# Kernel optimization log

Measured on AMD Instinct MI355X. Metric: run time of the kernel, lower is better.

## Reference

```python
import jax, jax.numpy as jnp
import numpy as np

N_NODES = 50000
N_EDGES = 800000
IN_DIM = 64
OUT_DIM = 128
K = 2
FINAL_DIM = IN_DIM * (2 ** (K + 1))  # 512


def _mean_agg(h, src, dst, inv_deg, n):
    # mean over neighbors: message h[src] summed into dst, normalized by in-degree
    s = jax.ops.segment_sum(h[src], dst, num_segments=n)
    return s * inv_deg[:, None]


def setup_inputs() -> dict:
    key = jax.random.key(0)
    k1, k2, k3 = jax.random.split(key, 3)
    feature = jax.random.normal(k1, (N_NODES, IN_DIM), dtype=jnp.float32)
    edge_index = jax.random.randint(k2, (2, N_EDGES), 0, N_NODES, dtype=jnp.int64)
    W = jax.random.normal(k3, (OUT_DIM, FINAL_DIM), dtype=jnp.float32) * 0.02
    b = jnp.zeros((OUT_DIM,), dtype=jnp.float32)
    return {"feature": feature, "edge_index": edge_index, "W": W, "b": b}


def reference(feature, edge_index, W, b):
    n = feature.shape[0]
    src, dst = edge_index[0], edge_index[1]
    ones = jnp.ones((src.shape[0],), dtype=feature.dtype)
    # degree normalizers (clamped to 1) for mean aggregation, each direction
    deg_in = jax.ops.segment_sum(ones, dst, num_segments=n)
    deg_out = jax.ops.segment_sum(ones, src, num_segments=n)
    inv_in = 1.0 / jnp.maximum(deg_in, 1.0)
    inv_out = 1.0 / jnp.maximum(deg_out, 1.0)

    h = feature
    for _ in range(K + 1):  # K+1 directed hops; dim doubles each hop
        h_in = _mean_agg(h, src, dst, inv_in, n)   # aggregate from in-neighbors
        h_out = _mean_agg(h, dst, src, inv_out, n)  # aggregate from out-neighbors
        h = jnp.concatenate([h_in, h_out], axis=-1)

    # output linear projection: [N, FINAL_DIM] @ [FINAL_DIM, OUT_DIM]
    return h @ W.T + b
```

## Files before the change

### kernel.cpp

```cpp
#include <hip/hip_runtime.h>

#define NN 50000
#define NE 800000
#define NBUCK 100
#define BUCK_N 500
#define CAP 10016
#define CAPS 9024
#define PA_BLOCKS 500
#define PA_CHUNK 1600

typedef __attribute__((ext_vector_type(8))) short short8;
typedef __attribute__((ext_vector_type(4))) float floatx4;

__device__ __forceinline__ unsigned short f2b(float x) {
    unsigned u = __float_as_uint(x);
    return (unsigned short)((u + 0x7fffu + ((u >> 16) & 1u)) >> 16);
}
__device__ __forceinline__ unsigned pk2(float lo, float hi) {
    return (unsigned)f2b(lo) | ((unsigned)f2b(hi) << 16);
}
__device__ __forceinline__ float blo(unsigned u) { return __uint_as_float(u << 16); }
__device__ __forceinline__ float bhi(unsigned u) { return __uint_as_float(u & 0xffff0000u); }
__device__ __forceinline__ void acc8(uint4 u, float* a) {
    a[0] += blo(u.x); a[1] += bhi(u.x);
    a[2] += blo(u.y); a[3] += bhi(u.y);
    a[4] += blo(u.z); a[5] += bhi(u.z);
    a[6] += blo(u.w); a[7] += bhi(u.w);
}

__global__ void prep_kernel(const float4* __restrict__ f32, uint2* __restrict__ fb,
                            const float* __restrict__ W, unsigned short* __restrict__ Bnk) {
    int bid = blockIdx.x;
    if (bid < 3125) {
        int idx = bid * 256 + threadIdx.x;
        float4 v = f32[idx];
        fb[idx] = make_uint2(pk2(v.x, v.y), pk2(v.z, v.w));
    } else {
        int idx = (bid - 3125) * 256 + threadIdx.x;
        int n = idx >> 8, k = idx & 255;
        float v = (n < 128) ? W[n * 512 + k] : W[(n - 128) * 512 + 256 + k];
        Bnk[idx] = f2b(v);
    }
}

__global__ __launch_bounds__(256) void bucket_kernel(const int* __restrict__ src,
                                                     const int* __restrict__ dst,
                                                     int* __restrict__ gcnt_in,
                                                     int* __restrict__ gcnt_out,
                                                     int2* __restrict__ pin,
                                                     int2* __restrict__ pout) {
    __shared__ int cin[NBUCK], cout[NBUCK], rin[NBUCK], rout[NBUCK];
    int tid = threadIdx.x;
    if (tid < NBUCK) { cin[tid] = 0; cout[tid] = 0; }
    __syncthreads();
    int e0 = blockIdx.x * PA_CHUNK, e1 = e0 + PA_CHUNK;
    for (int e = e0 + tid; e < e1; e += 256) {
        atomicAdd(&cin[dst[e] / BUCK_N], 1);
        atomicAdd(&cout[src[e] / BUCK_N], 1);
    }
    __syncthreads();
    if (tid < NBUCK) {
        rin[tid]  = atomicAdd(&gcnt_in[tid], cin[tid]);
        rout[tid] = atomicAdd(&gcnt_out[tid], cout[tid]);
        cin[tid] = 0; cout[tid] = 0;
    }
    __syncthreads();
    for (int e = e0 + tid; e < e1; e += 256) {
        int s = src[e], d = dst[e];
        int bi = d / BUCK_N;
        int p = atomicAdd(&cin[bi], 1);
        pin[(size_t)bi * CAP + rin[bi] + p] = make_int2(d, s);
        int bo = s / BUCK_N;
        int q = atomicAdd(&cout[bo], 1);
        pout[(size_t)bo * CAP + rout[bo] + q] = make_int2(s, d);
    }
}

__global__ void bucket_scan_kernel(const int* __restrict__ gcnt_in,
                                   const int* __restrict__ gcnt_out,
                                   int* __restrict__ bb_in, int* __restrict__ bb_out) {
    if (threadIdx.x == 0) {
        int run = 0;
        for (int b = 0; b < NBUCK; ++b) { bb_in[b] = run; run += gcnt_in[b]; }
    }
    if (threadIdx.x == 1) {
        int run = 0;
        for (int b = 0; b < NBUCK; ++b) { bb_out[b] = run; run += gcnt_out[b]; }
    }
}

__global__ __launch_bounds__(1024) void csr_build_kernel(const int2* __restrict__ pin,
                                                         const int2* __restrict__ pout,
                                                         const int* __restrict__ gcnt_in,
                                                         const int* __restrict__ gcnt_out,
                                                         const int* __restrict__ bb_in,
                                                         const int* __restrict__ bb_out,
                                                         int* __restrict__ row_in,
                                                         int* __restrict__ row_out,
                                                         int* __restrict__ csr_in,
                                                         int* __restrict__ csr_out) {
    bool dirout = blockIdx.x >= NBUCK;
    int b = dirout ? blockIdx.x - NBUCK : blockIdx.x;
    const int2* pairs = (dirout ? pout : pin) + (size_t)b * CAP;
    int cnt  = dirout ? gcnt_out[b] : gcnt_in[b];
    int base = dirout ? bb_out[b] : bb_in[b];
    int* row = dirout ? row_out : row_in;
    int* csr = dirout ? csr_out : csr_in;
    int lo = b * BUCK_N;
    __shared__ unsigned sbuf[CAPS];
    __shared__ int deg[BUCK_N], incl[BUCK_N], cur[BUCK_N];
    __shared__ int hnb[NBUCK], snb[NBUCK], cnb[NBUCK];
    int tid = threadIdx.x;
    if (tid < BUCK_N) { deg[tid] = 0; cur[tid] = 0; }
    if (tid < NBUCK) { hnb[tid] = 0; cnb[tid] = 0; }
    __syncthreads();
    for (int i = tid; i < cnt; i += 1024) {
        int2 pr = pairs[i];
        atomicAdd(&deg[pr.x - lo], 1);
        atomicAdd(&hnb[pr.y / BUCK_N], 1);
    }
    __syncthreads();
    if (tid < BUCK_N) incl[tid] = deg[tid];
    if (tid < NBUCK) snb[tid] = hnb[tid];
    __syncthreads();
    for (int off = 1; off < BUCK_N; off <<= 1) {
        int v = 0, w = 0;
        if (tid < BUCK_N && tid >= off) v = incl[tid - off];
        if (tid < NBUCK && tid >= off) w = snb[tid - off];
        __syncthreads();
        if (tid < BUCK_N) incl[tid] += v;
        if (tid < NBUCK && off < NBUCK) snb[tid] += w;
        __syncthreads();
    }
    if (tid < BUCK_N) row[lo + tid] = base + incl[tid] - deg[tid];
    if (tid == 0 && b == NBUCK - 1) row[NN] = base + incl[BUCK_N - 1];
    __syncthreads();
    if (cnt <= CAPS) {
        for (int i = tid; i < cnt; i += 1024) {
            int2 pr = pairs[i];
            int nb = pr.y / BUCK_N;
            int pos = snb[nb] - hnb[nb] + atomicAdd(&cnb[nb], 1);
            sbuf[pos] = ((unsigned)(pr.x - lo) << 17) | (unsigned)pr.y;
        }
        __syncthreads();
        for (int i = tid; i < cnt; i += 1024) {
            unsigned k = sbuf[i];
            int li = k >> 17;
            int pos = atomicAdd(&cur[li], 1);
            csr[base + incl[li] - deg[li] + pos] = (int)(k & 0x1FFFFu);
        }
    } else {
        for (int i = tid; i < cnt; i += 1024) {
            int2 pr = pairs[i];
            int li = pr.x - lo;
            int pos = atomicAdd(&cur[li], 1);
            csr[base + incl[li] - deg[li] + pos] = pr.y;
        }
    }
}

__global__ void gather1_kernel(const uint4* __restrict__ feat,
                               const int* __restrict__ row_in, const int* __restrict__ csr_in,
                               const int* __restrict__ row_out, const int* __restrict__ csr_out,
                               uint4* __restrict__ h1) {
    unsigned idx = blockIdx.x * 256 + threadIdx.x;
    unsigned n = idx >> 4, r = idx & 15;
    bool is_out = (r >= 8);
    unsigned f = r & 7;
    const int* row = is_out ? row_out : row_in;
    const int* csr = is_out ? csr_out : csr_in;
    int beg = row[n], end = row[n + 1];
    float inv = 1.0f / fmaxf((float)(end - beg), 1.0f);
    float a[8] = {};
    int j = beg;
    for (; j + 3 < end; j += 4) {
        uint4 u0 = feat[(size_t)csr[j] * 8 + f];
        uint4 u1 = feat[(size_t)csr[j + 1] * 8 + f];
        uint4 u2 = feat[(size_t)csr[j + 2] * 8 + f];
        uint4 u3 = feat[(size_t)csr[j + 3] * 8 + f];
        acc8(u0, a); acc8(u1, a); acc8(u2, a); acc8(u3, a);
    }
    for (; j < end; ++j) acc8(feat[(size_t)csr[j] * 8 + f], a);
    uint4 o;
    o.x = pk2(a[0] * inv, a[1] * inv);
    o.y = pk2(a[2] * inv, a[3] * inv);
    o.z = pk2(a[4] * inv, a[5] * inv);
    o.w = pk2(a[6] * inv, a[7] * inv);
    h1[(size_t)n * 16 + r] = o;
}

__global__ void gather2_kernel(const uint4* __restrict__ h1,
                               const int* __restrict__ row_in, const int* __restrict__ csr_in,
                               const int* __restrict__ row_out, const int* __restrict__ csr_out,
                               uint4* __restrict__ h2) {
    unsigned idx = blockIdx.x * 256 + threadIdx.x;
    unsigned n = idx >> 5, r = idx & 31;
    bool is_out = (r >= 16);
    unsigned f = r & 15;
    const int* row = is_out ? row_out : row_in;
    const int* csr = is_out ? csr_out : csr_in;
    int beg = row[n], end = row[n + 1];
    float inv = 1.0f / fmaxf((float)(end - beg), 1.0f);
    float a[8] = {};
    int j = beg;
    for (; j + 3 < end; j += 4) {
        uint4 u0 = h1[(size_t)csr[j] * 16 + f];
        uint4 u1 = h1[(size_t)csr[j + 1] * 16 + f];
        uint4 u2 = h1[(size_t)csr[j + 2] * 16 + f];
        uint4 u3 = h1[(size_t)csr[j + 3] * 16 + f];
        acc8(u0, a); acc8(u1, a); acc8(u2, a); acc8(u3, a);
    }
    for (; j < end; ++j) acc8(h1[(size_t)csr[j] * 16 + f], a);
    uint4 o;
    o.x = pk2(a[0] * inv, a[1] * inv);
    o.y = pk2(a[2] * inv, a[3] * inv);
    o.z = pk2(a[4] * inv, a[5] * inv);
    o.w = pk2(a[6] * inv, a[7] * inv);
    h2[(size_t)n * 32 + r] = o;
}

__global__ __launch_bounds__(256) void gemm_mfma_kernel(const unsigned short* __restrict__ A,
                                                        const unsigned short* __restrict__ Bnk,
                                                        unsigned short* __restrict__ C) {
    __shared__ unsigned short Bs[16][264];
    __shared__ unsigned short Cb[4][16][264];
    int tid = threadIdx.x;
    int wave = tid >> 6, lane = tid & 63;
    int l15 = lane & 15, q = lane >> 4;
    int m0 = blockIdx.x * 128;
    short8 af[2][8];
#pragma unroll
    for (int t = 0; t < 2; ++t) {
        int mrow = m0 + (wave + 4 * t) * 16 + l15;
        const unsigned short* Arow = A + (size_t)min(mrow, NN - 1) * 256;
#pragma unroll
        for (int s = 0; s < 8; ++s)
            af[t][s] = *(const short8*)(Arow + s * 32 + q * 8);
    }
    floatx4 acc[2][16];
#pragma unroll
    for (int t = 0; t < 2; ++t)
#pragma unroll
        for (int c = 0; c < 16; ++c) acc[t][c] = (floatx4){0.f, 0.f, 0.f, 0.f};
#pragma unroll
    for (int c = 0; c < 16; ++c) {
        {
            int nl = tid >> 4, seg = tid & 15;
            const uint4* srcp = (const uint4*)(Bnk + ((size_t)(16 * c + nl)) * 256 + seg * 16);
            uint4 v0 = srcp[0], v1 = srcp[1];
            *(uint4*)&Bs[nl][seg * 16] = v0;
            *(uint4*)&Bs[nl][seg * 16 + 8] = v1;
        }
        __syncthreads();
#pragma unroll
        for (int s = 0; s < 8; ++s) {
            short8 bf = *(const short8*)&Bs[l15][s * 32 + q * 8];
            acc[0][c] = __builtin_amdgcn_mfma_f32_16x16x32_bf16(af[0][s], bf, acc[0][c], 0, 0, 0);
            acc[1][c] = __builtin_amdgcn_mfma_f32_16x16x32_bf16(af[1][s], bf, acc[1][c], 0, 0, 0);
        }
        __syncthreads();
    }
#pragma unroll
    for (int t = 0; t < 2; ++t) {
#pragma unroll
        for (int c = 0; c < 16; ++c)
#pragma unroll
            for (int r = 0; r < 4; ++r)
                Cb[wave][q * 4 + r][16 * c + l15] = f2b(acc[t][c][r]);
        __syncthreads();
#pragma unroll
        for (int i = 0; i < 8; ++i) {
            int tt = i * 64 + lane;
            int rrow = tt >> 5;
            int seg = tt & 31;
            int m = m0 + (wave + 4 * t) * 16 + rrow;
            if (m < NN) {
                uint4 v = *(const uint4*)&Cb[wave][rrow][seg * 8];
                *(uint4*)(C + (size_t)m * 256 + seg * 8) = v;
            }
        }
        __syncthreads();
    }
}

__global__ void final_kernel(const uint4* __restrict__ g,
                             const int* __restrict__ row_in, const int* __restrict__ csr_in,
                             const int* __restrict__ row_out, const int* __restrict__ csr_out,
                             const float4* __restrict__ b4, float4* __restrict__ out) {
    unsigned idx = blockIdx.x * 256 + threadIdx.x;
    unsigned n = idx >> 4, f = idx & 15;
    float a[8] = {};
    {
        int beg = row_in[n], end = row_in[n + 1];
        float inv = 1.0f / fmaxf((float)(end - beg), 1.0f);
        float s[8] = {};
        int j = beg;
        for (; j + 3 < end; j += 4) {
            uint4 u0 = g[(size_t)csr_in[j] * 32 + f];
            uint4 u1 = g[(size_t)csr_in[j + 1] * 32 + f];
            uint4 u2 = g[(size_t)csr_in[j + 2] * 32 + f];
            uint4 u3 = g[(size_t)csr_in[j + 3] * 32 + f];
            acc8(u0, s); acc8(u1, s); acc8(u2, s); acc8(u3, s);
        }
        for (; j < end; ++j) acc8(g[(size_t)csr_in[j] * 32 + f], s);
#pragma unroll
        for (int i = 0; i < 8; ++i) a[i] += s[i] * inv;
    }
    {
        int beg = row_out[n], end = row_out[n + 1];
        float inv = 1.0f / fmaxf((float)(end - beg), 1.0f);
        float s[8] = {};
        int j = beg;
        for (; j + 3 < end; j += 4) {
            uint4 u0 = g[(size_t)csr_out[j] * 32 + 16 + f];
            uint4 u1 = g[(size_t)csr_out[j + 1] * 32 + 16 + f];
            uint4 u2 = g[(size_t)csr_out[j + 2] * 32 + 16 + f];
            uint4 u3 = g[(size_t)csr_out[j + 3] * 32 + 16 + f];
            acc8(u0, s); acc8(u1, s); acc8(u2, s); acc8(u3, s);
        }
        for (; j < end; ++j) acc8(g[(size_t)csr_out[j] * 32 + 16 + f], s);
#pragma unroll
        for (int i = 0; i < 8; ++i) a[i] += s[i] * inv;
    }
    float4 b0 = b4[2 * f], b1 = b4[2 * f + 1];
    out[(size_t)n * 32 + 2 * f]     = make_float4(a[0] + b0.x, a[1] + b0.y, a[2] + b0.z, a[3] + b0.w);
    out[(size_t)n * 32 + 2 * f + 1] = make_float4(a[4] + b1.x, a[5] + b1.y, a[6] + b1.z, a[7] + b1.w);
}

extern "C" void kernel_launch(void* const* d_in, const int* in_sizes, int n_in,
                              void* d_out, int out_size, void* d_ws, size_t ws_size,
                              hipStream_t stream) {
    const float* feature = (const float*)d_in[0];
    const int*   edges   = (const int*)d_in[1];
    const float* W       = (const float*)d_in[2];
    const float* b       = (const float*)d_in[3];
    const int* src = edges;
    const int* dst = edges + NE;
    float* out = (float*)d_out;

    unsigned short* featb = (unsigned short*)d_ws;
    unsigned short* h1b = featb + (size_t)NN * 64;
    unsigned short* h2b = h1b + (size_t)NN * 128;
    unsigned short* gb  = h2b + (size_t)NN * 256;
    unsigned short* Bnk = gb + (size_t)NN * 256;
    int2* pin  = (int2*)(Bnk + 65536);
    int2* pout = pin + (size_t)NBUCK * CAP;
    int* csr_in  = (int*)(pout + (size_t)NBUCK * CAP);
    int* csr_out = csr_in + NE;
    int* row_in  = csr_out + NE;
    int* row_out = row_in + NN + 1;
    int* gcnt_in  = row_out + NN + 1;
    int* gcnt_out = gcnt_in + 128;
    int* bb_in   = gcnt_out + 128;
    int* bb_out  = bb_in + 128;

    (void)hipMemsetAsync(gcnt_in, 0, 256 * sizeof(int), stream);
    prep_kernel<<<3125 + 256, 256, 0, stream>>>((const float4*)feature, (uint2*)featb, W, Bnk);
    bucket_kernel<<<PA_BLOCKS, 256, 0, stream>>>(src, dst, gcnt_in, gcnt_out, pin, pout);
    bucket_scan_kernel<<<1, 64, 0, stream>>>(gcnt_in, gcnt_out, bb_in, bb_out);
    csr_build_kernel<<<2 * NBUCK, 1024, 0, stream>>>(pin, pout, gcnt_in, gcnt_out,
                                                     bb_in, bb_out, row_in, row_out,
                                                     csr_in, csr_out);

    gather1_kernel<<<(NN * 16) / 256, 256, 0, stream>>>(
        (const uint4*)featb, row_in, csr_in, row_out, csr_out, (uint4*)h1b);
    gather2_kernel<<<(NN * 32) / 256, 256, 0, stream>>>(
        (const uint4*)h1b, row_in, csr_in, row_out, csr_out, (uint4*)h2b);
    gemm_mfma_kernel<<<(NN + 127) / 128, 256, 0, stream>>>(h2b, Bnk, gb);
    final_kernel<<<(NN * 16) / 256, 256, 0, stream>>>(
        (const uint4*)gb, row_in, csr_in, row_out, csr_out, (const float4*)b, (float4*)out);
}
```

Measured before the change: 274.0 us.

## Fuse second-hop gather into GEMM and drop scan kernel and memset

The second-hop neighbor gather now writes its bf16 rows into shared memory, and the MFMA projection reads them from there in the same kernel, so the h2 buffer is never written to or read back from global memory. The GEMM tile shrinks from 128 to 64 rows per block, so each block loads the weight tiles for only half as many rows. The separate bucket-scan kernel and the memset are removed: prep_kernel zeroes the counters, and each csr_build block sums its own prefix. This cuts two launches and a global round trip, at the cost of less B reuse per block and gather latency sitting in front of the MFMA work.

```diff
diff --git a/kernel.cpp b/kernel.cpp
--- a/kernel.cpp
+++ b/kernel.cpp
@@ -29,17 +29,20 @@
 }
 
 __global__ void prep_kernel(const float4* __restrict__ f32, uint2* __restrict__ fb,
-                            const float* __restrict__ W, unsigned short* __restrict__ Bnk) {
+                            const float* __restrict__ W, unsigned short* __restrict__ Bnk,
+                            int* __restrict__ gcnt) {
     int bid = blockIdx.x;
     if (bid < 3125) {
         int idx = bid * 256 + threadIdx.x;
         float4 v = f32[idx];
         fb[idx] = make_uint2(pk2(v.x, v.y), pk2(v.z, v.w));
-    } else {
+    } else if (bid < 3381) {
         int idx = (bid - 3125) * 256 + threadIdx.x;
         int n = idx >> 8, k = idx & 255;
         float v = (n < 128) ? W[n * 512 + k] : W[(n - 128) * 512 + 256 + k];
         Bnk[idx] = f2b(v);
+    } else {
+        gcnt[threadIdx.x] = 0;
     }
 }
 
@@ -76,25 +79,10 @@
     }
 }
 
-__global__ void bucket_scan_kernel(const int* __restrict__ gcnt_in,
-                                   const int* __restrict__ gcnt_out,
-                                   int* __restrict__ bb_in, int* __restrict__ bb_out) {
-    if (threadIdx.x == 0) {
-        int run = 0;
-        for (int b = 0; b < NBUCK; ++b) { bb_in[b] = run; run += gcnt_in[b]; }
-    }
-    if (threadIdx.x == 1) {
-        int run = 0;
-        for (int b = 0; b < NBUCK; ++b) { bb_out[b] = run; run += gcnt_out[b]; }
-    }
-}
-
 __global__ __launch_bounds__(1024) void csr_build_kernel(const int2* __restrict__ pin,
                                                          const int2* __restrict__ pout,
                                                          const int* __restrict__ gcnt_in,
                                                          const int* __restrict__ gcnt_out,
-                                                         const int* __restrict__ bb_in,
-                                                         const int* __restrict__ bb_out,
                                                          int* __restrict__ row_in,
                                                          int* __restrict__ row_out,
                                                          int* __restrict__ csr_in,
@@ -102,8 +90,10 @@
     bool dirout = blockIdx.x >= NBUCK;
     int b = dirout ? blockIdx.x - NBUCK : blockIdx.x;
     const int2* pairs = (dirout ? pout : pin) + (size_t)b * CAP;
-    int cnt  = dirout ? gcnt_out[b] : gcnt_in[b];
-    int base = dirout ? bb_out[b] : bb_in[b];
+    const int* gcnt = dirout ? gcnt_out : gcnt_in;
+    int cnt = gcnt[b];
+    int base = 0;
+    for (int i = 0; i < b; ++i) base += gcnt[i];
     int* row = dirout ? row_out : row_in;
     int* csr = dirout ? csr_out : csr_in;
     int lo = b * BUCK_N;
@@ -189,59 +179,60 @@
     h1[(size_t)n * 16 + r] = o;
 }
 
-__global__ void gather2_kernel(const uint4* __restrict__ h1,
-                               const int* __restrict__ row_in, const int* __restrict__ csr_in,
-                               const int* __restrict__ row_out, const int* __restrict__ csr_out,
-                               uint4* __restrict__ h2) {
-    unsigned idx = blockIdx.x * 256 + threadIdx.x;
-    unsigned n = idx >> 5, r = idx & 31;
-    bool is_out = (r >= 16);
-    unsigned f = r & 15;
-    const int* row = is_out ? row_out : row_in;
-    const int* csr = is_out ? csr_out : csr_in;
-    int beg = row[n], end = row[n + 1];
-    float inv = 1.0f / fmaxf((float)(end - beg), 1.0f);
-    float a[8] = {};
-    int j = beg;
-    for (; j + 3 < end; j += 4) {
-        uint4 u0 = h1[(size_t)csr[j] * 16 + f];
-        uint4 u1 = h1[(size_t)csr[j + 1] * 16 + f];
-        uint4 u2 = h1[(size_t)csr[j + 2] * 16 + f];
-        uint4 u3 = h1[(size_t)csr[j + 3] * 16 + f];
-        acc8(u0, a); acc8(u1, a); acc8(u2, a); acc8(u3, a);
-    }
-    for (; j < end; ++j) acc8(h1[(size_t)csr[j] * 16 + f], a);
-    uint4 o;
-    o.x = pk2(a[0] * inv, a[1] * inv);
-    o.y = pk2(a[2] * inv, a[3] * inv);
-    o.z = pk2(a[4] * inv, a[5] * inv);
-    o.w = pk2(a[6] * inv, a[7] * inv);
-    h2[(size_t)n * 32 + r] = o;
-}
-
-__global__ __launch_bounds__(256) void gemm_mfma_kernel(const unsigned short* __restrict__ A,
-                                                        const unsigned short* __restrict__ Bnk,
-                                                        unsigned short* __restrict__ C) {
+__global__ __launch_bounds__(256) void g2gemm_kernel(const uint4* __restrict__ h1,
+                                                     const int* __restrict__ row_in,
+                                                     const int* __restrict__ csr_in,
+                                                     const int* __restrict__ row_out,
+                                                     const int* __restrict__ csr_out,
+                                                     const unsigned short* __restrict__ Bnk,
+                                                     unsigned short* __restrict__ g) {
+    __shared__ unsigned short pool[64 * 264];
     __shared__ unsigned short Bs[16][264];
-    __shared__ unsigned short Cb[4][16][264];
     int tid = threadIdx.x;
     int wave = tid >> 6, lane = tid & 63;
     int l15 = lane & 15, q = lane >> 4;
-    int m0 = blockIdx.x * 128;
-    short8 af[2][8];
-#pragma unroll
-    for (int t = 0; t < 2; ++t) {
-        int mrow = m0 + (wave + 4 * t) * 16 + l15;
-        const unsigned short* Arow = A + (size_t)min(mrow, NN - 1) * 256;
-#pragma unroll
-        for (int s = 0; s < 8; ++s)
-            af[t][s] = *(const short8*)(Arow + s * 32 + q * 8);
-    }
-    floatx4 acc[2][16];
-#pragma unroll
-    for (int t = 0; t < 2; ++t)
-#pragma unroll
-        for (int c = 0; c < 16; ++c) acc[t][c] = (floatx4){0.f, 0.f, 0.f, 0.f};
+    int m0 = blockIdx.x * 64;
+
+    {
+        int r = tid & 31;
+        bool is_out = (r >= 16);
+        unsigned f = r & 15;
+        const int* row = is_out ? row_out : row_in;
+        const int* csr = is_out ? csr_out : csr_in;
+        for (int grp = 0; grp < 8; ++grp) {
+            int ln = grp * 8 + (tid >> 5);
+            int n = m0 + ln;
+            uint4 o = make_uint4(0u, 0u, 0u, 0u);
+            if (n < NN) {
+                int beg = row[n], end = row[n + 1];
+                float inv = 1.0f / fmaxf((float)(end - beg), 1.0f);
+                float a[8] = {};
+                int j = beg;
+                for (; j + 3 < end; j += 4) {
+                    uint4 u0 = h1[(size_t)csr[j] * 16 + f];
+                    uint4 u1 = h1[(size_t)csr[j + 1] * 16 + f];
+                    uint4 u2 = h1[(size_t)csr[j + 2] * 16 + f];
+                    uint4 u3 = h1[(size_t)csr[j + 3] * 16 + f];
+                    acc8(u0, a); acc8(u1, a); acc8(u2, a); acc8(u3, a);
+                }
+                for (; j < end; ++j) acc8(h1[(size_t)csr[j] * 16 + f], a);
+                o.x = pk2(a[0] * inv, a[1] * inv);
+                o.y = pk2(a[2] * inv, a[3] * inv);
+                o.z = pk2(a[4] * inv, a[5] * inv);
+                o.w = pk2(a[6] * inv, a[7] * inv);
+            }
+            *(uint4*)&pool[ln * 264 + r * 8] = o;
+        }
+    }
+    __syncthreads();
+
+    short8 af[8];
+#pragma unroll
+    for (int s = 0; s < 8; ++s)
+        af[s] = *(const short8*)&pool[(wave * 16 + l15) * 264 + s * 32 + q * 8];
+    floatx4 acc[16];
+#pragma unroll
+    for (int c = 0; c < 16; ++c) acc[c] = (floatx4){0.f, 0.f, 0.f, 0.f};
 #pragma unroll
     for (int c = 0; c < 16; ++c) {
         {
@@ -255,31 +246,27 @@
 #pragma unroll
         for (int s = 0; s < 8; ++s) {
             short8 bf = *(const short8*)&Bs[l15][s * 32 + q * 8];
-            acc[0][c] = __builtin_amdgcn_mfma_f32_16x16x32_bf16(af[0][s], bf, acc[0][c], 0, 0, 0);
-            acc[1][c] = __builtin_amdgcn_mfma_f32_16x16x32_bf16(af[1][s], bf, acc[1][c], 0, 0, 0);
-        }
-        __syncthreads();
-    }
-#pragma unroll
-    for (int t = 0; t < 2; ++t) {
-#pragma unroll
-        for (int c = 0; c < 16; ++c)
-#pragma unroll
-            for (int r = 0; r < 4; ++r)
-                Cb[wave][q * 4 + r][16 * c + l15] = f2b(acc[t][c][r]);
-        __syncthreads();
-#pragma unroll
-        for (int i = 0; i < 8; ++i) {
-            int tt = i * 64 + lane;
-            int rrow = tt >> 5;
-            int seg = tt & 31;
-            int m = m0 + (wave + 4 * t) * 16 + rrow;
-            if (m < NN) {
-                uint4 v = *(const uint4*)&Cb[wave][rrow][seg * 8];
-                *(uint4*)(C + (size_t)m * 256 + seg * 8) = v;
-            }
-        }
-        __syncthreads();
+            acc[c] = __builtin_amdgcn_mfma_f32_16x16x32_bf16(af[s], bf, acc[c], 0, 0, 0);
+        }
+        __syncthreads();
+    }
+    unsigned short* Cw = pool + wave * 16 * 264;
+#pragma unroll
+    for (int c = 0; c < 16; ++c)
+#pragma unroll
+        for (int rr = 0; rr < 4; ++rr)
+            Cw[(q * 4 + rr) * 264 + 16 * c + l15] = f2b(acc[c][rr]);
+    __syncthreads();
+#pragma unroll
+    for (int i = 0; i < 8; ++i) {
+        int t = i * 64 + lane;
+        int rrow = t >> 5;
+        int seg = t & 31;
+        int m = m0 + wave * 16 + rrow;
+        if (m < NN) {
+            uint4 v = *(const uint4*)&Cw[rrow * 264 + seg * 8];
+            *(uint4*)(g + (size_t)m * 256 + seg * 8) = v;
+        }
     }
 }
 
@@ -340,8 +327,7 @@
 
     unsigned short* featb = (unsigned short*)d_ws;
     unsigned short* h1b = featb + (size_t)NN * 64;
-    unsigned short* h2b = h1b + (size_t)NN * 128;
-    unsigned short* gb  = h2b + (size_t)NN * 256;
+    unsigned short* gb  = h1b + (size_t)NN * 128;
     unsigned short* Bnk = gb + (size_t)NN * 256;
     int2* pin  = (int2*)(Bnk + 65536);
     int2* pout = pin + (size_t)NBUCK * CAP;
@@ -351,22 +337,15 @@
     int* row_out = row_in + NN + 1;
     int* gcnt_in  = row_out + NN + 1;
     int* gcnt_out = gcnt_in + 128;
-    int* bb_in   = gcnt_out + 128;
-    int* bb_out  = bb_in + 128;
-
-    (void)hipMemsetAsync(gcnt_in, 0, 256 * sizeof(int), stream);
-    prep_kernel<<<3125 + 256, 256, 0, stream>>>((const float4*)feature, (uint2*)featb, W, Bnk);
+
+    prep_kernel<<<3382, 256, 0, stream>>>((const float4*)feature, (uint2*)featb, W, Bnk, gcnt_in);
     bucket_kernel<<<PA_BLOCKS, 256, 0, stream>>>(src, dst, gcnt_in, gcnt_out, pin, pout);
-    bucket_scan_kernel<<<1, 64, 0, stream>>>(gcnt_in, gcnt_out, bb_in, bb_out);
     csr_build_kernel<<<2 * NBUCK, 1024, 0, stream>>>(pin, pout, gcnt_in, gcnt_out,
-                                                     bb_in, bb_out, row_in, row_out,
-                                                     csr_in, csr_out);
-
+                                                     row_in, row_out, csr_in, csr_out);
     gather1_kernel<<<(NN * 16) / 256, 256, 0, stream>>>(
         (const uint4*)featb, row_in, csr_in, row_out, csr_out, (uint4*)h1b);
-    gather2_kernel<<<(NN * 32) / 256, 256, 0, stream>>>(
-        (const uint4*)h1b, row_in, csr_in, row_out, csr_out, (uint4*)h2b);
-    gemm_mfma_kernel<<<(NN + 127) / 128, 256, 0, stream>>>(h2b, Bnk, gb);
+    g2gemm_kernel<<<(NN + 63) / 64, 256, 0, stream>>>(
+        (const uint4*)h1b, row_in, csr_in, row_out, csr_out, Bnk, gb);
     final_kernel<<<(NN * 16) / 256, 256, 0, stream>>>(
         (const uint4*)gb, row_in, csr_in, row_out, csr_out, (const float4*)b, (float4*)out);
 }
```

New measurement: 304.2 us. +11.0%, slower.
